# Kernel tuning notes

Measured on AMD Instinct MI355X. Metric: run time of the kernel, lower is better.

The kernel has to match this reference:

```python
import jax, jax.numpy as jnp
import numpy as np

DECAY = 0.99
EPS_VQ = 1e-5
EPS_LN = 1e-5


def setup_inputs() -> dict:
    key = jax.random.key(0)
    ks = jax.random.split(key, 6)
    N, DIN, D, K = 32768, 1024, 512, 1024
    return {
        "x": jax.random.normal(ks[0], (N, DIN), dtype=jnp.float32),
        "enc_w": jax.random.normal(ks[1], (DIN, D), dtype=jnp.float32) * (1.0 / np.sqrt(DIN)),
        "enc_b": jnp.zeros((D,), jnp.float32),
        "ln_g": jnp.ones((D,), jnp.float32),
        "ln_b": jnp.zeros((D,), jnp.float32),
        "dec_w": jax.random.normal(ks[2], (D, DIN), dtype=jnp.float32) * (1.0 / np.sqrt(D)),
        "dec_b": jnp.zeros((DIN,), jnp.float32),
        "embeddings": jax.random.normal(ks[3], (K, D), dtype=jnp.float32),
        "cluster_size": jnp.ones((K,), jnp.float32),
        "ema_embed_sum": jax.random.normal(ks[4], (K, D), dtype=jnp.float32),
    }


def _layernorm(h, g, b):
    mu = jnp.mean(h, axis=-1, keepdims=True)
    var = jnp.var(h, axis=-1, keepdims=True)
    return (h - mu) * jax.lax.rsqrt(var + EPS_LN) * g + b


def reference(x, enc_w, enc_b, ln_g, ln_b, dec_w, dec_b, embeddings, cluster_size, ema_embed_sum):
    K = embeddings.shape[0]
    # encoder: Linear + LayerNorm
    z_e = _layernorm(x @ enc_w + enc_b, ln_g, ln_b)  # [N, D]
    # pairwise squared L2 distances, expanded GEMM form (same argmin as (z-e)^2.sum)
    d = (jnp.sum(z_e * z_e, axis=1, keepdims=True)
         - 2.0 * (z_e @ embeddings.T)
         + jnp.sum(embeddings * embeddings, axis=1)[None, :])  # [N, K]
    indices = jnp.argmin(d, axis=1)  # [N]
    z_q = embeddings[indices]  # gather [N, D]
    # EMA codebook update (training path; buffers, no grad)
    zd = jax.lax.stop_gradient(z_e)
    counts = jax.ops.segment_sum(jnp.ones_like(indices, jnp.float32), indices, num_segments=K)
    embed_sum = jax.ops.segment_sum(zd, indices, num_segments=K)  # one_hot.T @ z
    new_cluster_size = DECAY * cluster_size + (1.0 - DECAY) * counts
    new_ema_embed_sum = DECAY * ema_embed_sum + (1.0 - DECAY) * embed_sum
    n = jnp.sum(new_cluster_size)
    cs = (new_cluster_size + EPS_VQ) / (n + K * EPS_VQ) * n
    new_embeddings = new_ema_embed_sum / cs[:, None]
    # commitment loss + straight-through estimator
    commit_loss = jnp.mean((z_e - jax.lax.stop_gradient(z_q)) ** 2)
    z_q_st = z_e + jax.lax.stop_gradient(z_q - z_e)
    x_recon = z_q_st @ dec_w + dec_b
    return (x_recon, commit_loss, indices, z_e, z_q_st,
            new_embeddings, new_cluster_size, new_ema_embed_sum)
```

## Files before the change

### kernel.cpp

```cpp
#include <hip/hip_runtime.h>

typedef unsigned long long u64;
typedef unsigned int u32;
typedef _Float16 f16;
typedef _Float16 f16x8 __attribute__((ext_vector_type(8)));
typedef float f32x4 __attribute__((ext_vector_type(4)));

#define MFMA16(a, b, c) __builtin_amdgcn_mfma_f32_16x16x32_f16(a, b, c, 0, 0, 0)

#define NROWS 32768
#define DIN   1024
#define DM    512
#define KC    1024
#define SPLIT_SC  1024.0f
#define SPLIT_INV 0.0009765625f
#define CHSZ  32
#define MAXCH 2048
#define MARGIN 0.5f

#define OFF_XR   0ull
#define OFF_CL   33554432ull
#define OFF_IDX  33554433ull
#define OFF_ZE   33587201ull
#define OFF_ZQ   50364417ull
#define OFF_NE   67141633ull
#define OFF_NCS  67665921ull
#define OFF_NEMA 67666945ull

#define WS_ZNORM   2359296ull
#define WS_IDX     2490368ull
#define WS_COUNTS  2621440ull
#define WS_STARTS  2625536ull
#define WS_OFFW    2629632ull
#define WS_ROWLIST 2633728ull
#define WS_CSD     2764800ull
#define WS_ENORM   2769920ull
#define WS2_CAND   (4ull<<20)
#define WS2_WT1    (36ull<<20)
#define WS2_WT2    (37ull<<20)
#define WS2_DT     (38ull<<20)
#define WS2_E1     (39ull<<20)
#define WS3_CHPFX  (41ull<<20)
#define WS3_CHCODE ((41ull<<20) + 8192)
#define WS3_CPART  ((41ull<<20) + 16384)
#define WS3_PART   ((41ull<<20) + 65536)

__device__ inline void gload16(const f16* g, f16* l) {
  __builtin_amdgcn_global_load_lds((const __attribute__((address_space(1))) void*)g,
                                   (__attribute__((address_space(3))) void*)l, 16, 0, 0);
}

__device__ inline f16x8 ldfrag32(const f16* p, int row, int kc) {
  return *(const f16x8*)(p + row * 32 + ((kc ^ ((row >> 1) & 3)) << 3));
}
__device__ inline f16x8 ldfrag64(const f16* p, int row, int kc) {
  return *(const f16x8*)(p + row * 64 + ((kc ^ (row & 7)) << 3));
}

__device__ inline void stage32(const f16* gbase, int ld, int row0, int k0,
                               f16* lds, int t) {
  int r = t >> 2, c = t & 3;
  int cs = c ^ ((r >> 1) & 3);
  gload16(gbase + (size_t)(row0 + r) * ld + k0 + cs * 8, lds + t * 8);
}

__device__ inline void stage64(const f16* gbase, int ld, int row0, int k0,
                               f16* lds, int t) {
#pragma unroll
  for (int h = 0; h < 2; h++) {
    int e = t + h * 512;
    int r = e >> 3, c = e & 7;
    int cs = c ^ (r & 7);
    gload16(gbase + (size_t)(row0 + r) * ld + k0 + cs * 8, lds + e * 8);
  }
}

#define BAR1_V4   { asm volatile("s_waitcnt vmcnt(4)" ::: "memory"); \
                    __builtin_amdgcn_sched_barrier(0); \
                    __builtin_amdgcn_s_barrier(); \
                    asm volatile("" ::: "memory"); }
#define BAR1_V0L0 { asm volatile("s_waitcnt vmcnt(0) lgkmcnt(0)" ::: "memory"); \
                    __builtin_amdgcn_sched_barrier(0); \
                    __builtin_amdgcn_s_barrier(); \
                    asm volatile("" ::: "memory"); }
#define BAR2      { asm volatile("s_waitcnt lgkmcnt(0)" ::: "memory"); \
                    __builtin_amdgcn_s_barrier(); \
                    asm volatile("" ::: "memory"); }

__device__ inline u32 enc_score(float s) {
  u32 kb = __float_as_uint(s);
  return (kb & 0x80000000u) ? ~kb : (kb | 0x80000000u);
}
__device__ inline float dec_score(u32 u) {
  u32 b = (u & 0x80000000u) ? (u & 0x7fffffffu) : ~u;
  return __uint_as_float(b);
}

__global__ __launch_bounds__(256) void k_prep(const float* __restrict__ enc_w,
                                              const float* __restrict__ dec_w,
                                              const float* __restrict__ emb,
                                              f16* __restrict__ wt1,
                                              f16* __restrict__ wt2,
                                              f16* __restrict__ dT,
                                              f16* __restrict__ e1,
                                              float* __restrict__ enorm,
                                              int* __restrict__ counts) {
  __shared__ float tile[32][33];
  int bid = blockIdx.x, t = threadIdx.x;
  if (bid < 1024) {
    const float* W;
    f16 *o1, *o2;
    int K, N, bx, by;
    if (bid < 512) {
      W = enc_w; o1 = wt1; o2 = wt2; K = DIN; N = DM;
      bx = bid & 15; by = bid >> 4;
    } else {
      int b2 = bid - 512;
      W = dec_w; o1 = dT; o2 = nullptr; K = DM; N = DIN;
      bx = b2 & 31; by = b2 >> 5;
    }
    int tx = t & 31, ty = t >> 5;
    int nb = bx * 32, kb = by * 32;
#pragma unroll
    for (int i = 0; i < 32; i += 8)
      tile[ty + i][tx] = W[(size_t)(kb + ty + i) * N + nb + tx];
    __syncthreads();
#pragma unroll
    for (int i = 0; i < 32; i += 8) {
      float v = tile[tx][ty + i];
      f16 h = (f16)v;
      size_t o = (size_t)(nb + ty + i) * K + kb + tx;
      o1[o] = h;
      if (o2) o2[o] = (f16)((v - (float)h) * SPLIT_SC);
    }
  } else if (bid < 1536) {
    int tid = (bid - 1024) * 256 + t;
    for (int i = tid; i < KC * DM; i += 131072) e1[i] = (f16)emb[i];
  } else if (bid < 1792) {
    int k = (bid - 1536) * 4 + (t >> 6), lane = t & 63;
    float s = 0.f;
#pragma unroll
    for (int j = 0; j < 8; j++) {
      float v = emb[(size_t)k * DM + lane + j * 64];
      s = fmaf(v, v, s);
    }
#pragma unroll
    for (int m = 1; m < 64; m <<= 1) s += __shfl_xor(s, m, 64);
    if (lane == 0) enorm[k] = s;
  } else {
    int i = (bid - 1792) * 256 + t;
    if (i < KC) counts[i] = 0;
  }
}

__global__ __launch_bounds__(512) void k_genc4(const float* __restrict__ x,
                                               const f16* __restrict__ wt1,
                                               const f16* __restrict__ wt2,
                                               const float* __restrict__ bias,
                                               float* __restrict__ dst) {
  __shared__ __align__(16) f16 A1[128 * 32], A2[128 * 32];
  __shared__ __align__(16) f16 B1[2][128 * 32], B2[2][128 * 32];
  int t = threadIdx.x, lane = t & 63, wid = t >> 6;
  int wm = wid >> 2, wn = wid & 3;
  int l = blockIdx.x;
  int xcd = l & 7, s = l >> 3, ct = s & 3;
  int p = ((s >> 2) << 3) | xcd;
  int m0 = p * 128, n0 = ct * 128;
  int r = t >> 2, cg = t & 3;
  int cslot = cg ^ ((r >> 1) & 3);
  const float* ax = x + (size_t)(m0 + r) * DIN + cg * 8;
  f32x4 accA[4][2] = {}, accB[4][2] = {};

#define GCONV(v0, v1)                                                       \
  {                                                                         \
    float a_[8] = {v0.x, v0.y, v0.z, v0.w, v1.x, v1.y, v1.z, v1.w};         \
    f16 h1_[8], h2_[8];                                                     \
    _Pragma("unroll") for (int j_ = 0; j_ < 8; j_++) {                      \
      f16 h_ = (f16)a_[j_];                                                 \
      h1_[j_] = h_;                                                         \
      h2_[j_] = (f16)((a_[j_] - (float)h_) * SPLIT_SC);                     \
    }                                                                       \
    *(f16x8*)(A1 + r * 32 + cslot * 8) = *(f16x8*)h1_;                      \
    *(f16x8*)(A2 + r * 32 + cslot * 8) = *(f16x8*)h2_;                      \
  }

#define GCOMP(buf)                                                          \
  {                                                                         \
    int kc_ = lane >> 4;                                                    \
    f16x8 a1f[4], a2f[4], b1f[2], b2f[2];                                   \
    _Pragma("unroll") for (int m_ = 0; m_ < 4; m_++) {                      \
      int row_ = wm * 64 + m_ * 16 + (lane & 15);                           \
      a1f[m_] = ldfrag32(A1, row_, kc_);                                    \
      a2f[m_] = ldfrag32(A2, row_, kc_);                                    \
    }                                                                       \
    _Pragma("unroll") for (int n_ = 0; n_ < 2; n_++) {                      \
      int row_ = wn * 32 + n_ * 16 + (lane & 15);                           \
      b1f[n_] = ldfrag32(B1[buf], row_, kc_);                               \
      b2f[n_] = ldfrag32(B2[buf], row_, kc_);                               \
    }                                                                       \
    _Pragma("unroll") for (int m_ = 0; m_ < 4; m_++)                        \
      _Pragma("unroll") for (int n_ = 0; n_ < 2; n_++) {                    \
        accA[m_][n_] = MFMA16(a1f[m_], b1f[n_], accA[m_][n_]);              \
        accB[m_][n_] = MFMA16(a1f[m_], b2f[n_], accB[m_][n_]);              \
        accB[m_][n_] = MFMA16(a2f[m_], b1f[n_], accB[m_][n_]);              \
      }                                                                     \
  }

  float4 c0 = *(const float4*)(ax);
  float4 c1 = *(const float4*)(ax + 4);
  float4 n0v = *(const float4*)(ax + 32);
  float4 n1v = *(const float4*)(ax + 36);
  stage32(wt1, DIN, n0, 0, B1[0], t);
  stage32(wt2, DIN, n0, 0, B2[0], t);
  asm volatile("s_waitcnt vmcnt(4)" ::: "memory");

  for (int it = 0; it < 32; ++it) {
    GCONV(c0, c1);
    if (it + 1 < 32) {
      stage32(wt1, DIN, n0, (it + 1) * 32, B1[(it + 1) & 1], t);
      stage32(wt2, DIN, n0, (it + 1) * 32, B2[(it + 1) & 1], t);
    }
    float4 f0, f1;
    if (it + 2 < 32) {
      f0 = *(const float4*)(ax + (it + 2) * 32);
      f1 = *(const float4*)(ax + (it + 2) * 32 + 4);
    }
    if (it <= 29) {
      asm volatile("s_waitcnt vmcnt(4) lgkmcnt(0)" ::: "memory");
    } else if (it == 30) {
      asm volatile("s_waitcnt vmcnt(2) lgkmcnt(0)" ::: "memory");
    } else {
      asm volatile("s_waitcnt vmcnt(0) lgkmcnt(0)" ::: "memory");
    }
    __builtin_amdgcn_sched_barrier(0);
    __builtin_amdgcn_s_barrier();
    asm volatile("" ::: "memory");
    GCOMP(it & 1);
    BAR2;
    c0 = n0v; c1 = n1v; n0v = f0; n1v = f1;
  }
#undef GCONV
#undef GCOMP

#pragma unroll
  for (int m = 0; m < 4; m++)
#pragma unroll
    for (int n = 0; n < 2; n++)
#pragma unroll
      for (int j = 0; j < 4; j++) {
        int row = m0 + wm * 64 + m * 16 + (lane >> 4) * 4 + j;
        int col = n0 + wn * 32 + n * 16 + (lane & 15);
        dst[(size_t)row * DM + col] = accA[m][n][j] + SPLIT_INV * accB[m][n][j] + bias[col];
      }
}

__global__ __launch_bounds__(512) void k_dist3(const f16* __restrict__ z1,
                                               const f16* __restrict__ e1,
                                               const float* __restrict__ enorm,
                                               u64* __restrict__ cand) {
  __shared__ __align__(16) f16 A1[2][128 * 64], B1[2][128 * 64];
  __shared__ u64 cand_s[128][8];
  int t = threadIdx.x, lane = t & 63, wid = t >> 6;
  int wm = wid >> 2, wn = wid & 3;
  int l = blockIdx.x;
  int xcd = l & 7, s = l >> 3, ct = s & 7;
  int p = ((s >> 3) << 3) | xcd;
  int r0 = p * 128, c0 = ct * 128;
  f32x4 acc[4][2] = {};

  stage64(z1, DM, r0, 0, A1[0], t);
  stage64(e1, DM, c0, 0, B1[0], t);
  int cur = 0;

  for (int it = 0; it < 8; ++it) {
    if (it < 7) {
      int k0n = (it + 1) * 64;
      stage64(z1, DM, r0, k0n, A1[cur ^ 1], t);
      stage64(e1, DM, c0, k0n, B1[cur ^ 1], t);
      BAR1_V4;
    } else {
      BAR1_V0L0;
    }
#pragma unroll
    for (int kk = 0; kk < 2; kk++) {
      int kc = kk * 4 + (lane >> 4);
      f16x8 a1f[4], b1f[2];
#pragma unroll
      for (int m = 0; m < 4; m++)
        a1f[m] = ldfrag64(A1[cur], wm * 64 + m * 16 + (lane & 15), kc);
#pragma unroll
      for (int n = 0; n < 2; n++)
        b1f[n] = ldfrag64(B1[cur], wn * 32 + n * 16 + (lane & 15), kc);
#pragma unroll
      for (int m = 0; m < 4; m++)
#pragma unroll
        for (int n = 0; n < 2; n++) acc[m][n] = MFMA16(a1f[m], b1f[n], acc[m][n]);
    }
    BAR2;
    cur ^= 1;
  }

  float en0 = enorm[c0 + wn * 32 + (lane & 15)];
  float en1 = enorm[c0 + wn * 32 + 16 + (lane & 15)];
#pragma unroll
  for (int m = 0; m < 4; m++)
#pragma unroll
    for (int j = 0; j < 4; j++) {
      int r_l = wm * 64 + m * 16 + (lane >> 4) * 4 + j;
      int col0 = c0 + wn * 32 + (lane & 15);
      float s0 = fmaf(-2.0f, acc[m][0][j], en0);
      float s1 = fmaf(-2.0f, acc[m][1][j], en1);
      u64 k0 = ((u64)enc_score(s0) << 32) | (u32)col0;
      u64 k1 = ((u64)enc_score(s1) << 32) | (u32)(col0 + 16);
      u64 lo = k0 < k1 ? k0 : k1;
      u64 hi = k0 < k1 ? k1 : k0;
#pragma unroll
      for (int msk = 1; msk < 16; msk <<= 1) {
        u64 lo2 = __shfl_xor(lo, msk, 64);
        u64 hi2 = __shfl_xor(hi, msk, 64);
        u64 nlo = lo < lo2 ? lo : lo2;
        u64 losr = lo < lo2 ? lo2 : lo;
        u64 nh = hi < hi2 ? hi : hi2;
        hi = losr < nh ? losr : nh;
        lo = nlo;
      }
      if ((lane & 15) == 0) {
        cand_s[r_l][wn * 2] = lo;
        cand_s[r_l][wn * 2 + 1] = hi;
      }
    }
  __syncthreads();
  if (t < 128) {
    u64 b0 = ~0ull, b1 = ~0ull;
#pragma unroll
    for (int i = 0; i < 8; i++) {
      u64 k = cand_s[t][i];
      if (k < b0) { b1 = b0; b0 = k; }
      else if (k < b1) { b1 = k; }
    }
    u64* dst = cand + ((size_t)(r0 + t) * 16 + ct * 2);
    dst[0] = b0;
    dst[1] = b1;
  }
}

__global__ __launch_bounds__(256) void k_resolve(const u64* __restrict__ cand,
                                                 const float* __restrict__ znorm,
                                                 const float* __restrict__ enorm,
                                                 const float* __restrict__ emb,
                                                 float* __restrict__ out,
                                                 int* __restrict__ idxws,
                                                 int* __restrict__ counts,
                                                 float* __restrict__ cpart) {
  int t = threadIdx.x, bid = blockIdx.x;
  int r0 = bid * 16;
  __shared__ u64 key_s[256];
  __shared__ int idx_s[16];
  __shared__ float commit_s[16];
  __shared__ int flagcnt_s;
  __shared__ int flagrow_s[16];
  key_s[t] = cand[(size_t)r0 * 16 + t];
  if (t == 0) flagcnt_s = 0;
  __syncthreads();

  if (t < 16) {
    u64 best = ~0ull;
#pragma unroll
    for (int i = 0; i < 16; i++) {
      u64 k = key_s[t * 16 + i];
      best = k < best ? k : best;
    }
    float smin = dec_score((u32)(best >> 32));
    float thr = smin + MARGIN;
    int nc = 0;
#pragma unroll
    for (int i = 0; i < 16; i++)
      if (dec_score((u32)(key_s[t * 16 + i] >> 32)) <= thr) nc++;
    idx_s[t] = (int)(u32)(best & 0xffffffffull);
    commit_s[t] = znorm[r0 + t] + smin;
    if (nc > 1) {
      int pz = atomicAdd(&flagcnt_s, 1);
      flagrow_s[pz] = t;
    }
  }
  __syncthreads();

  if (t < 64) {
    int nf = flagcnt_s;
    for (int fi = 0; fi < nf; fi++) {
      int lr = flagrow_s[fi];
      int R = r0 + lr;
      u64 amin = ~0ull;
      for (int i = 0; i < 16; i++) {
        u64 k = key_s[lr * 16 + i];
        amin = k < amin ? k : amin;
      }
      float thr = dec_score((u32)(amin >> 32)) + MARGIN;
      float zn = znorm[R];
      const float* z = out + OFF_ZE + (size_t)R * DM;
      u64 bestk = ~0ull;
      for (int i = 0; i < 16; i++) {
        u64 k = key_s[lr * 16 + i];
        if (dec_score((u32)(k >> 32)) > thr) continue;
        int c = (int)(u32)(k & 0xffffffffull);
        const float* e = emb + (size_t)c * DM;
        float pdot = 0.f;
#pragma unroll
        for (int j = 0; j < 8; j++) pdot = fmaf(z[t + j * 64], e[t + j * 64], pdot);
#pragma unroll
        for (int m = 1; m < 64; m <<= 1) pdot += __shfl_xor(pdot, m, 64);
        float d = fmaf(-2.0f, pdot, zn) + enorm[c];
        u64 pk = ((u64)enc_score(d) << 32) | (u32)c;
        bestk = pk < bestk ? pk : bestk;
      }
      if (t == 0) {
        idx_s[lr] = (int)(u32)(bestk & 0xffffffffull);
        commit_s[lr] = dec_score((u32)(bestk >> 32));
      }
    }
  }
  __syncthreads();

  if (t < 16) {
    int R = r0 + t;
    int idx = idx_s[t];
    out[OFF_IDX + R] = (float)idx;
    idxws[R] = idx;
    atomicAdd(counts + idx, 1);
  }
  __syncthreads();
  for (int rr = 0; rr < 16; rr++) {
    int R = r0 + rr;
    const float* e = emb + (size_t)idx_s[rr] * DM;
    float* zq = out + OFF_ZQ + (size_t)R * DM;
#pragma unroll
    for (int j = 0; j < 2; j++) {
      int c = t + j * 256;
      zq[c] = e[c];
    }
  }
  if (t == 0) {
    float s = 0.f;
#pragma unroll
    for (int i = 0; i < 16; i++) s += commit_s[i];
    cpart[bid] = s;
  }
}

__global__ __launch_bounds__(512) void k_gdec3(const f16* __restrict__ e1,
                                               const int* __restrict__ idxws,
                                               const f16* __restrict__ dT,
                                               const float* __restrict__ bias,
                                               float* __restrict__ dst) {
  __shared__ __align__(16) f16 A1[2][128 * 64], B1[2][128 * 64];
  int t = threadIdx.x, lane = t & 63, wid = t >> 6;
  int wm = wid >> 2, wn = wid & 3;
  int l = blockIdx.x;
  int xcd = l & 7, s = l >> 3, ct = s & 7;
  int p = ((s >> 3) << 3) | xcd;
  int m0 = p * 128, n0 = ct * 128;
  f32x4 acc[4][2] = {};

  int ra = t >> 3;
  int cs = (t & 7) ^ (ra & 7);
  int ia = idxws[m0 + ra];
  int ib = idxws[m0 + 64 + ra];
  const f16* pa = e1 + (size_t)ia * DM + cs * 8;
  const f16* pb = e1 + (size_t)ib * DM + cs * 8;

  gload16(pa, A1[0] + t * 8);
  gload16(pb, A1[0] + (t + 512) * 8);
  stage64(dT, DM, n0, 0, B1[0], t);
  int cur = 0;

  for (int it = 0; it < 8; ++it) {
    if (it < 7) {
      int k0n = (it + 1) * 64;
      gload16(pa + k0n, A1[cur ^ 1] + t * 8);
      gload16(pb + k0n, A1[cur ^ 1] + (t + 512) * 8);
      stage64(dT, DM, n0, k0n, B1[cur ^ 1], t);
      BAR1_V4;
    } else {
      BAR1_V0L0;
    }
#pragma unroll
    for (int kk = 0; kk < 2; kk++) {
      int kc = kk * 4 + (lane >> 4);
      f16x8 a1f[4], b1f[2];
#pragma unroll
      for (int m = 0; m < 4; m++)
        a1f[m] = ldfrag64(A1[cur], wm * 64 + m * 16 + (lane & 15), kc);
#pragma unroll
      for (int n = 0; n < 2; n++)
        b1f[n] = ldfrag64(B1[cur], wn * 32 + n * 16 + (lane & 15), kc);
#pragma unroll
      for (int m = 0; m < 4; m++)
#pragma unroll
        for (int n = 0; n < 2; n++) acc[m][n] = MFMA16(a1f[m], b1f[n], acc[m][n]);
    }
    BAR2;
    cur ^= 1;
  }
#pragma unroll
  for (int m = 0; m < 4; m++)
#pragma unroll
    for (int n = 0; n < 2; n++)
#pragma unroll
      for (int j = 0; j < 4; j++) {
        int row = m0 + wm * 64 + m * 16 + (lane >> 4) * 4 + j;
        int col = n0 + wn * 32 + n * 16 + (lane & 15);
        dst[(size_t)row * DIN + col] = acc[m][n][j] + bias[col];
      }
}

__global__ __launch_bounds__(256) void k_ln3(float* __restrict__ ze,
                                             const float* __restrict__ g,
                                             const float* __restrict__ b,
                                             f16* __restrict__ z1,
                                             float* __restrict__ znorm) {
  int t = threadIdx.x, lane = t & 63, wid = t >> 6;
  int R = blockIdx.x * 4 + wid;
  float* row = ze + (size_t)R * DM;
  float v[8];
  float s = 0.f, sq = 0.f;
#pragma unroll
  for (int j = 0; j < 8; j++) {
    v[j] = row[lane + j * 64];
    s += v[j];
    sq = fmaf(v[j], v[j], sq);
  }
#pragma unroll
  for (int m = 1; m < 64; m <<= 1) {
    s += __shfl_xor(s, m, 64);
    sq += __shfl_xor(sq, m, 64);
  }
  float mu = s * (1.f / DM);
  float var = sq * (1.f / DM) - mu * mu;
  float rs = rsqrtf(var + 1e-5f);
  float zn = 0.f;
#pragma unroll
  for (int j = 0; j < 8; j++) {
    int c = lane + j * 64;
    float o = (v[j] - mu) * rs * g[c] + b[c];
    row[c] = o;
    z1[(size_t)R * DM + c] = (f16)o;
    zn = fmaf(o, o, zn);
  }
#pragma unroll
  for (int m = 1; m < 64; m <<= 1) zn += __shfl_xor(zn, m, 64);
  if (lane == 0) znorm[R] = zn;
}

__global__ __launch_bounds__(1024) void k_scan(const int* __restrict__ counts,
                                               const float* __restrict__ cs_in,
                                               float* __restrict__ out,
                                               int* __restrict__ starts,
                                               int* __restrict__ offw,
                                               float* __restrict__ csd,
                                               const float* __restrict__ cpart,
                                               int* __restrict__ chpfx,
                                               int* __restrict__ chcode) {
  __shared__ float f[1024];
  __shared__ int ib[1024];
  int t = threadIdx.x;
  f[t] = cpart[t] + cpart[t + 1024];
  __syncthreads();
  for (int s = 512; s > 0; s >>= 1) {
    if (t < s) f[t] += f[t + s];
    __syncthreads();
  }
  if (t == 0) out[OFF_CL] = f[0] * (1.f / ((float)NROWS * (float)DM));
  __syncthreads();

  int cnt = counts[t];
  float ncs = 0.99f * cs_in[t] + 0.01f * (float)cnt;
  out[OFF_NCS + t] = ncs;
  f[t] = ncs;
  __syncthreads();
  for (int s = 512; s > 0; s >>= 1) {
    if (t < s) f[t] += f[t + s];
    __syncthreads();
  }
  float n = f[0];
  csd[t] = (ncs + 1e-5f) / (n + (float)KC * 1e-5f) * n;
  ib[t] = cnt;
  __syncthreads();
  for (int s = 1; s < 1024; s <<= 1) {
    int y = (t >= s) ? ib[t - s] : 0;
    __syncthreads();
    ib[t] += y;
    __syncthreads();
  }
  int excl = ib[t] - cnt;
  starts[t] = excl;
  offw[t] = excl;
  int nch = (cnt + CHSZ - 1) / CHSZ;
  __syncthreads();
  ib[t] = nch;
  __syncthreads();
  for (int s = 1; s < 1024; s <<= 1) {
    int y = (t >= s) ? ib[t - s] : 0;
    __syncthreads();
    ib[t] += y;
    __syncthreads();
  }
  int chx = ib[t] - nch;
  chpfx[t] = chx;
  if (t == KC - 1) chpfx[KC] = ib[t];
  for (int j = 0; j < nch; j++) chcode[chx + j] = t;
}

__global__ __launch_bounds__(256) void k_scatter(const int* __restrict__ idxws,
                                                 int* __restrict__ offw,
                                                 int* __restrict__ rowlist) {
  int r = blockIdx.x * 256 + threadIdx.x;
  int idx = idxws[r];
  int pos = atomicAdd(offw + idx, 1);
  rowlist[pos] = r;
}

__global__ __launch_bounds__(128) void k_partsum(const int* __restrict__ chpfx,
                                                 const int* __restrict__ chcode,
                                                 const int* __restrict__ starts,
                                                 const int* __restrict__ counts,
                                                 const int* __restrict__ rowlist,
                                                 const float* __restrict__ out,
                                                 float* __restrict__ part) {
  int c = blockIdx.x, t = threadIdx.x;
  if (c >= chpfx[KC]) return;
  int code = chcode[c];
  int j = c - chpfx[code];
  int ofs = starts[code] + j * CHSZ;
  int len = min(CHSZ, counts[code] - j * CHSZ);
  __shared__ int rl[CHSZ];
  if (t < len) rl[t] = rowlist[ofs + t];
  __syncthreads();
  const float* zeb = out + OFF_ZE;
  float a0 = 0.f, a1 = 0.f, a2 = 0.f, a3 = 0.f;
  for (int i = 0; i < len; i++) {
    const float* z = zeb + (size_t)rl[i] * DM;
    a0 += z[t];
    a1 += z[t + 128];
    a2 += z[t + 256];
    a3 += z[t + 384];
  }
  float* pp = part + (size_t)c * DM;
  pp[t] = a0;
  pp[t + 128] = a1;
  pp[t + 256] = a2;
  pp[t + 384] = a3;
}

__global__ __launch_bounds__(128) void k_codesum2(const int* __restrict__ chpfx,
                                                  const float* __restrict__ part,
                                                  const float* __restrict__ ema_in,
                                                  const float* __restrict__ csd,
                                                  float* __restrict__ out) {
  int k = blockIdx.x, t = threadIdx.x;
  int base = chpfx[k], nch = chpfx[k + 1] - base;
  float a0 = 0.f, a1 = 0.f, a2 = 0.f, a3 = 0.f;
  for (int i = 0; i < nch; i++) {
    const float* pp = part + (size_t)(base + i) * DM;
    a0 += pp[t];
    a1 += pp[t + 128];
    a2 += pp[t + 256];
    a3 += pp[t + 384];
  }
  float cs = csd[k];
  float sum[4] = {a0, a1, a2, a3};
#pragma unroll
  for (int j = 0; j < 4; j++) {
    int c = t + j * 128;
    float e = 0.99f * ema_in[(size_t)k * DM + c] + 0.01f * sum[j];
    out[OFF_NEMA + (size_t)k * DM + c] = e;
    out[OFF_NE + (size_t)k * DM + c] = e / cs;
  }
}

extern "C" void kernel_launch(void* const* d_in, const int* in_sizes, int n_in,
                              void* d_out, int out_size, void* d_ws, size_t ws_size,
                              hipStream_t stream) {
  (void)in_sizes; (void)n_in; (void)out_size; (void)ws_size;
  const float* x = (const float*)d_in[0];
  const float* enc_w = (const float*)d_in[1];
  const float* enc_b = (const float*)d_in[2];
  const float* ln_g = (const float*)d_in[3];
  const float* ln_b = (const float*)d_in[4];
  const float* dec_w = (const float*)d_in[5];
  const float* dec_b = (const float*)d_in[6];
  const float* emb = (const float*)d_in[7];
  const float* cs_in = (const float*)d_in[8];
  const float* ema_in = (const float*)d_in[9];
  float* out = (float*)d_out;
  char* ws = (char*)d_ws;
  float* znorm = (float*)(ws + WS_ZNORM);
  int* idxws = (int*)(ws + WS_IDX);
  int* counts = (int*)(ws + WS_COUNTS);
  int* starts = (int*)(ws + WS_STARTS);
  int* offw = (int*)(ws + WS_OFFW);
  int* rowlist = (int*)(ws + WS_ROWLIST);
  float* csd = (float*)(ws + WS_CSD);
  float* enorm = (float*)(ws + WS_ENORM);
  u64* cand = (u64*)(ws + WS2_CAND);
  f16* wt1 = (f16*)(ws + WS2_WT1);
  f16* wt2 = (f16*)(ws + WS2_WT2);
  f16* dT = (f16*)(ws + WS2_DT);
  f16* e1 = (f16*)(ws + WS2_E1);
  int* chpfx = (int*)(ws + WS3_CHPFX);
  int* chcode = (int*)(ws + WS3_CHCODE);
  float* cpart = (float*)(ws + WS3_CPART);
  float* part = (float*)(ws + WS3_PART);
  f16* z1 = (f16*)out;

  k_prep<<<dim3(1796), dim3(256), 0, stream>>>(enc_w, dec_w, emb, wt1, wt2, dT,
                                               e1, enorm, counts);
  k_genc4<<<dim3(1024), dim3(512), 0, stream>>>(x, wt1, wt2, enc_b, out + OFF_ZE);
  k_ln3<<<dim3(8192), dim3(256), 0, stream>>>(out + OFF_ZE, ln_g, ln_b, z1, znorm);
  k_dist3<<<dim3(2048), dim3(512), 0, stream>>>(z1, e1, enorm, cand);
  k_resolve<<<dim3(2048), dim3(256), 0, stream>>>(cand, znorm, enorm, emb, out,
                                                  idxws, counts, cpart);
  k_scan<<<dim3(1), dim3(1024), 0, stream>>>(counts, cs_in, out, starts, offw, csd,
                                             cpart, chpfx, chcode);
  k_scatter<<<dim3(NROWS / 256), dim3(256), 0, stream>>>(idxws, offw, rowlist);
  k_partsum<<<dim3(MAXCH), dim3(128), 0, stream>>>(chpfx, chcode, starts, counts,
                                                   rowlist, out, part);
  k_codesum2<<<dim3(KC), dim3(128), 0, stream>>>(chpfx, part, ema_in, csd, out);
  k_gdec3<<<dim3(2048), dim3(512), 0, stream>>>(e1, idxws, dT, dec_b, out + OFF_XR);
}
```

Before: 368.6 us.

## Load encoder A fragments directly into registers, dropping shared-memory A staging

The encoder GEMM now has each wave own 16 rows across all 128 columns. Each wave loads and converts its x slice straight into MFMA A fragments in registers, so the A tiles no longer go through LDS and lgkmcnt waits on A are removed. It also sets launch_bounds occupancy to 4 waves per SIMD. In exchange, each B fragment is read from LDS by all 8 waves rather than 4, which raises LDS read traffic per MFMA, and global x loads follow the fragment layout instead of the previous coalesced pattern.

```diff
diff --git a/kernel.cpp b/kernel.cpp
--- a/kernel.cpp
+++ b/kernel.cpp
@@ -153,25 +153,23 @@
   }
 }
 
-__global__ __launch_bounds__(512) void k_genc4(const float* __restrict__ x,
-                                               const f16* __restrict__ wt1,
-                                               const f16* __restrict__ wt2,
-                                               const float* __restrict__ bias,
-                                               float* __restrict__ dst) {
-  __shared__ __align__(16) f16 A1[128 * 32], A2[128 * 32];
+__global__ __launch_bounds__(512, 4) void k_genc5(const float* __restrict__ x,
+                                                  const f16* __restrict__ wt1,
+                                                  const f16* __restrict__ wt2,
+                                                  const float* __restrict__ bias,
+                                                  float* __restrict__ dst) {
   __shared__ __align__(16) f16 B1[2][128 * 32], B2[2][128 * 32];
   int t = threadIdx.x, lane = t & 63, wid = t >> 6;
-  int wm = wid >> 2, wn = wid & 3;
   int l = blockIdx.x;
   int xcd = l & 7, s = l >> 3, ct = s & 3;
   int p = ((s >> 2) << 3) | xcd;
-  int m0 = p * 128, n0 = ct * 128;
-  int r = t >> 2, cg = t & 3;
-  int cslot = cg ^ ((r >> 1) & 3);
-  const float* ax = x + (size_t)(m0 + r) * DIN + cg * 8;
-  f32x4 accA[4][2] = {}, accB[4][2] = {};
-
-#define GCONV(v0, v1)                                                       \
+  int m0 = p * 128, nc0 = ct * 128;
+  int kc = lane >> 4;
+  const float* ax = x + (size_t)(m0 + wid * 16 + (lane & 15)) * DIN + kc * 8;
+  f32x4 accA[8] = {}, accB[8] = {};
+  f16x8 a1f, a2f;
+
+#define GCONV5(v0, v1)                                                      \
   {                                                                         \
     float a_[8] = {v0.x, v0.y, v0.z, v0.w, v1.x, v1.y, v1.z, v1.w};         \
     f16 h1_[8], h2_[8];                                                     \
@@ -180,45 +178,23 @@
       h1_[j_] = h_;                                                         \
       h2_[j_] = (f16)((a_[j_] - (float)h_) * SPLIT_SC);                     \
     }                                                                       \
-    *(f16x8*)(A1 + r * 32 + cslot * 8) = *(f16x8*)h1_;                      \
-    *(f16x8*)(A2 + r * 32 + cslot * 8) = *(f16x8*)h2_;                      \
-  }
-
-#define GCOMP(buf)                                                          \
-  {                                                                         \
-    int kc_ = lane >> 4;                                                    \
-    f16x8 a1f[4], a2f[4], b1f[2], b2f[2];                                   \
-    _Pragma("unroll") for (int m_ = 0; m_ < 4; m_++) {                      \
-      int row_ = wm * 64 + m_ * 16 + (lane & 15);                           \
-      a1f[m_] = ldfrag32(A1, row_, kc_);                                    \
-      a2f[m_] = ldfrag32(A2, row_, kc_);                                    \
-    }                                                                       \
-    _Pragma("unroll") for (int n_ = 0; n_ < 2; n_++) {                      \
-      int row_ = wn * 32 + n_ * 16 + (lane & 15);                           \
-      b1f[n_] = ldfrag32(B1[buf], row_, kc_);                               \
-      b2f[n_] = ldfrag32(B2[buf], row_, kc_);                               \
-    }                                                                       \
-    _Pragma("unroll") for (int m_ = 0; m_ < 4; m_++)                        \
-      _Pragma("unroll") for (int n_ = 0; n_ < 2; n_++) {                    \
-        accA[m_][n_] = MFMA16(a1f[m_], b1f[n_], accA[m_][n_]);              \
-        accB[m_][n_] = MFMA16(a1f[m_], b2f[n_], accB[m_][n_]);              \
-        accB[m_][n_] = MFMA16(a2f[m_], b1f[n_], accB[m_][n_]);              \
-      }                                                                     \
+    a1f = *(f16x8*)h1_;                                                     \
+    a2f = *(f16x8*)h2_;                                                     \
   }
 
   float4 c0 = *(const float4*)(ax);
   float4 c1 = *(const float4*)(ax + 4);
+  stage32(wt1, DIN, nc0, 0, B1[0], t);
+  stage32(wt2, DIN, nc0, 0, B2[0], t);
   float4 n0v = *(const float4*)(ax + 32);
   float4 n1v = *(const float4*)(ax + 36);
-  stage32(wt1, DIN, n0, 0, B1[0], t);
-  stage32(wt2, DIN, n0, 0, B2[0], t);
   asm volatile("s_waitcnt vmcnt(4)" ::: "memory");
 
   for (int it = 0; it < 32; ++it) {
-    GCONV(c0, c1);
+    GCONV5(c0, c1);
     if (it + 1 < 32) {
-      stage32(wt1, DIN, n0, (it + 1) * 32, B1[(it + 1) & 1], t);
-      stage32(wt2, DIN, n0, (it + 1) * 32, B2[(it + 1) & 1], t);
+      stage32(wt1, DIN, nc0, (it + 1) * 32, B1[(it + 1) & 1], t);
+      stage32(wt2, DIN, nc0, (it + 1) * 32, B2[(it + 1) & 1], t);
     }
     float4 f0, f1;
     if (it + 2 < 32) {
@@ -226,32 +202,40 @@
       f1 = *(const float4*)(ax + (it + 2) * 32 + 4);
     }
     if (it <= 29) {
-      asm volatile("s_waitcnt vmcnt(4) lgkmcnt(0)" ::: "memory");
+      asm volatile("s_waitcnt vmcnt(4)" ::: "memory");
     } else if (it == 30) {
-      asm volatile("s_waitcnt vmcnt(2) lgkmcnt(0)" ::: "memory");
+      asm volatile("s_waitcnt vmcnt(2)" ::: "memory");
     } else {
-      asm volatile("s_waitcnt vmcnt(0) lgkmcnt(0)" ::: "memory");
+      asm volatile("s_waitcnt vmcnt(0)" ::: "memory");
     }
     __builtin_amdgcn_sched_barrier(0);
     __builtin_amdgcn_s_barrier();
     asm volatile("" ::: "memory");
-    GCOMP(it & 1);
+    {
+      const f16* bp1 = B1[it & 1];
+      const f16* bp2 = B2[it & 1];
+#pragma unroll
+      for (int n = 0; n < 8; n++) {
+        f16x8 b1f = ldfrag32(bp1, n * 16 + (lane & 15), kc);
+        f16x8 b2f = ldfrag32(bp2, n * 16 + (lane & 15), kc);
+        accA[n] = MFMA16(a1f, b1f, accA[n]);
+        accB[n] = MFMA16(a1f, b2f, accB[n]);
+        accB[n] = MFMA16(a2f, b1f, accB[n]);
+      }
+    }
     BAR2;
     c0 = n0v; c1 = n1v; n0v = f0; n1v = f1;
   }
-#undef GCONV
-#undef GCOMP
-
-#pragma unroll
-  for (int m = 0; m < 4; m++)
-#pragma unroll
-    for (int n = 0; n < 2; n++)
-#pragma unroll
-      for (int j = 0; j < 4; j++) {
-        int row = m0 + wm * 64 + m * 16 + (lane >> 4) * 4 + j;
-        int col = n0 + wn * 32 + n * 16 + (lane & 15);
-        dst[(size_t)row * DM + col] = accA[m][n][j] + SPLIT_INV * accB[m][n][j] + bias[col];
-      }
+#undef GCONV5
+
+#pragma unroll
+  for (int n = 0; n < 8; n++)
+#pragma unroll
+    for (int j = 0; j < 4; j++) {
+      int row = m0 + wid * 16 + (lane >> 4) * 4 + j;
+      int col = nc0 + n * 16 + (lane & 15);
+      dst[(size_t)row * DM + col] = accA[n][j] + SPLIT_INV * accB[n][j] + bias[col];
+    }
 }
 
 __global__ __launch_bounds__(512) void k_dist3(const f16* __restrict__ z1,
@@ -714,7 +698,7 @@
 
   k_prep<<<dim3(1796), dim3(256), 0, stream>>>(enc_w, dec_w, emb, wt1, wt2, dT,
                                                e1, enorm, counts);
-  k_genc4<<<dim3(1024), dim3(512), 0, stream>>>(x, wt1, wt2, enc_b, out + OFF_ZE);
+  k_genc5<<<dim3(1024), dim3(512), 0, stream>>>(x, wt1, wt2, enc_b, out + OFF_ZE);
   k_ln3<<<dim3(8192), dim3(256), 0, stream>>>(out + OFF_ZE, ln_g, ln_b, z1, znorm);
   k_dist3<<<dim3(2048), dim3(512), 0, stream>>>(z1, e1, enorm, cand);
   k_resolve<<<dim3(2048), dim3(256), 0, stream>>>(cand, znorm, enorm, emb, out,
```

Measured after the change: 386.5 us. 4.8% more time.

## Use 256x128 tiles with triple-buffered k32 pipeline for distance and decoder GEMMs

Applied to the files above, without the earlier changes.

Replaces the 128x128 double-buffered distance and decoder GEMM kernels with 256x128 tiles. Each wave now computes a 64x64 sub-tile, and a three-stage LDS ring with 32-wide K steps needs only one barrier per iteration. This raises arithmetic intensity per loaded byte, halves the block count, and removes the second barrier. In exchange it uses more LDS and registers per block, which may reduce occupancy, and makes the K loop longer with less work per step.

```diff
diff --git a/kernel.cpp b/kernel.cpp
--- a/kernel.cpp
+++ b/kernel.cpp
@@ -53,9 +53,6 @@
 __device__ inline f16x8 ldfrag32(const f16* p, int row, int kc) {
   return *(const f16x8*)(p + row * 32 + ((kc ^ ((row >> 1) & 3)) << 3));
 }
-__device__ inline f16x8 ldfrag64(const f16* p, int row, int kc) {
-  return *(const f16x8*)(p + row * 64 + ((kc ^ (row & 7)) << 3));
-}
 
 __device__ inline void stage32(const f16* gbase, int ld, int row0, int k0,
                                f16* lds, int t) {
@@ -64,25 +61,17 @@
   gload16(gbase + (size_t)(row0 + r) * ld + k0 + cs * 8, lds + t * 8);
 }
 
-__device__ inline void stage64(const f16* gbase, int ld, int row0, int k0,
-                               f16* lds, int t) {
+__device__ inline void stageA256(const f16* gbase, int ld, int row0, int k0,
+                                 f16* lds, int t) {
 #pragma unroll
   for (int h = 0; h < 2; h++) {
     int e = t + h * 512;
-    int r = e >> 3, c = e & 7;
-    int cs = c ^ (r & 7);
+    int r = e >> 2, c = e & 3;
+    int cs = c ^ ((r >> 1) & 3);
     gload16(gbase + (size_t)(row0 + r) * ld + k0 + cs * 8, lds + e * 8);
   }
 }
 
-#define BAR1_V4   { asm volatile("s_waitcnt vmcnt(4)" ::: "memory"); \
-                    __builtin_amdgcn_sched_barrier(0); \
-                    __builtin_amdgcn_s_barrier(); \
-                    asm volatile("" ::: "memory"); }
-#define BAR1_V0L0 { asm volatile("s_waitcnt vmcnt(0) lgkmcnt(0)" ::: "memory"); \
-                    __builtin_amdgcn_sched_barrier(0); \
-                    __builtin_amdgcn_s_barrier(); \
-                    asm volatile("" ::: "memory"); }
 #define BAR2      { asm volatile("s_waitcnt lgkmcnt(0)" ::: "memory"); \
                     __builtin_amdgcn_s_barrier(); \
                     asm volatile("" ::: "memory"); }
@@ -254,66 +243,71 @@
       }
 }
 
-__global__ __launch_bounds__(512) void k_dist3(const f16* __restrict__ z1,
-                                               const f16* __restrict__ e1,
-                                               const float* __restrict__ enorm,
-                                               u64* __restrict__ cand) {
-  __shared__ __align__(16) f16 A1[2][128 * 64], B1[2][128 * 64];
-  __shared__ u64 cand_s[128][8];
+__global__ __launch_bounds__(512, 4) void k_dist4(const f16* __restrict__ z1,
+                                                  const f16* __restrict__ e1,
+                                                  const float* __restrict__ enorm,
+                                                  u64* __restrict__ cand) {
+  __shared__ __align__(16) f16 A[3][256 * 32];
+  __shared__ __align__(16) f16 B[3][128 * 32];
   int t = threadIdx.x, lane = t & 63, wid = t >> 6;
-  int wm = wid >> 2, wn = wid & 3;
+  int wr = wid >> 1, wc = wid & 1;
   int l = blockIdx.x;
   int xcd = l & 7, s = l >> 3, ct = s & 7;
   int p = ((s >> 3) << 3) | xcd;
-  int r0 = p * 128, c0 = ct * 128;
-  f32x4 acc[4][2] = {};
-
-  stage64(z1, DM, r0, 0, A1[0], t);
-  stage64(e1, DM, c0, 0, B1[0], t);
-  int cur = 0;
-
-  for (int it = 0; it < 8; ++it) {
-    if (it < 7) {
-      int k0n = (it + 1) * 64;
-      stage64(z1, DM, r0, k0n, A1[cur ^ 1], t);
-      stage64(e1, DM, c0, k0n, B1[cur ^ 1], t);
-      BAR1_V4;
+  int r0 = p * 256, c0 = ct * 128;
+  f32x4 acc[4][4] = {};
+  int kc = lane >> 4;
+
+  stageA256(z1, DM, r0, 0, A[0], t);
+  stage32(e1, DM, c0, 0, B[0], t);
+
+  for (int it = 0; it < 16; ++it) {
+    int buf = it % 3;
+    if (it < 15) {
+      int nb = (it + 1) % 3;
+      int k0n = (it + 1) * 32;
+      stageA256(z1, DM, r0, k0n, A[nb], t);
+      stage32(e1, DM, c0, k0n, B[nb], t);
+      asm volatile("s_waitcnt vmcnt(3)" ::: "memory");
     } else {
-      BAR1_V0L0;
-    }
-#pragma unroll
-    for (int kk = 0; kk < 2; kk++) {
-      int kc = kk * 4 + (lane >> 4);
-      f16x8 a1f[4], b1f[2];
-#pragma unroll
-      for (int m = 0; m < 4; m++)
-        a1f[m] = ldfrag64(A1[cur], wm * 64 + m * 16 + (lane & 15), kc);
-#pragma unroll
-      for (int n = 0; n < 2; n++)
-        b1f[n] = ldfrag64(B1[cur], wn * 32 + n * 16 + (lane & 15), kc);
-#pragma unroll
-      for (int m = 0; m < 4; m++)
-#pragma unroll
-        for (int n = 0; n < 2; n++) acc[m][n] = MFMA16(a1f[m], b1f[n], acc[m][n]);
-    }
-    BAR2;
-    cur ^= 1;
-  }
-
-  float en0 = enorm[c0 + wn * 32 + (lane & 15)];
-  float en1 = enorm[c0 + wn * 32 + 16 + (lane & 15)];
+      asm volatile("s_waitcnt vmcnt(0)" ::: "memory");
+    }
+    __builtin_amdgcn_sched_barrier(0);
+    __builtin_amdgcn_s_barrier();
+    asm volatile("" ::: "memory");
+    f16x8 af[4], bf[4];
+#pragma unroll
+    for (int m = 0; m < 4; m++)
+      af[m] = ldfrag32(A[buf], wr * 64 + m * 16 + (lane & 15), kc);
+#pragma unroll
+    for (int n = 0; n < 4; n++)
+      bf[n] = ldfrag32(B[buf], wc * 64 + n * 16 + (lane & 15), kc);
+#pragma unroll
+    for (int m = 0; m < 4; m++)
+#pragma unroll
+      for (int n = 0; n < 4; n++) acc[m][n] = MFMA16(af[m], bf[n], acc[m][n]);
+  }
+
+  __syncthreads();
+  u64 (*cand_s)[4] = (u64 (*)[4])(&A[0][0]);
+  float en[4];
+#pragma unroll
+  for (int n = 0; n < 4; n++)
+    en[n] = enorm[c0 + wc * 64 + n * 16 + (lane & 15)];
 #pragma unroll
   for (int m = 0; m < 4; m++)
 #pragma unroll
     for (int j = 0; j < 4; j++) {
-      int r_l = wm * 64 + m * 16 + (lane >> 4) * 4 + j;
-      int col0 = c0 + wn * 32 + (lane & 15);
-      float s0 = fmaf(-2.0f, acc[m][0][j], en0);
-      float s1 = fmaf(-2.0f, acc[m][1][j], en1);
-      u64 k0 = ((u64)enc_score(s0) << 32) | (u32)col0;
-      u64 k1 = ((u64)enc_score(s1) << 32) | (u32)(col0 + 16);
-      u64 lo = k0 < k1 ? k0 : k1;
-      u64 hi = k0 < k1 ? k1 : k0;
+      int r_l = wr * 64 + m * 16 + (lane >> 4) * 4 + j;
+      u64 lo = ~0ull, hi = ~0ull;
+#pragma unroll
+      for (int n = 0; n < 4; n++) {
+        int col = c0 + wc * 64 + n * 16 + (lane & 15);
+        float sc = fmaf(-2.0f, acc[m][n][j], en[n]);
+        u64 k = ((u64)enc_score(sc) << 32) | (u32)col;
+        if (k < lo) { hi = lo; lo = k; }
+        else if (k < hi) { hi = k; }
+      }
 #pragma unroll
       for (int msk = 1; msk < 16; msk <<= 1) {
         u64 lo2 = __shfl_xor(lo, msk, 64);
@@ -325,15 +319,15 @@
         lo = nlo;
       }
       if ((lane & 15) == 0) {
-        cand_s[r_l][wn * 2] = lo;
-        cand_s[r_l][wn * 2 + 1] = hi;
+        cand_s[r_l][wc * 2] = lo;
+        cand_s[r_l][wc * 2 + 1] = hi;
       }
     }
   __syncthreads();
-  if (t < 128) {
+  if (t < 256) {
     u64 b0 = ~0ull, b1 = ~0ull;
 #pragma unroll
-    for (int i = 0; i < 8; i++) {
+    for (int i = 0; i < 4; i++) {
       u64 k = cand_s[t][i];
       if (k < b0) { b1 = b0; b0 = k; }
       else if (k < b1) { b1 = k; }
@@ -342,6 +336,73 @@
     dst[0] = b0;
     dst[1] = b1;
   }
+}
+
+__global__ __launch_bounds__(512, 4) void k_gdec4(const f16* __restrict__ e1,
+                                                  const int* __restrict__ idxws,
+                                                  const f16* __restrict__ dT,
+                                                  const float* __restrict__ bias,
+                                                  float* __restrict__ dst) {
+  __shared__ __align__(16) f16 A[3][256 * 32];
+  __shared__ __align__(16) f16 B[3][128 * 32];
+  int t = threadIdx.x, lane = t & 63, wid = t >> 6;
+  int wr = wid >> 1, wc = wid & 1;
+  int l = blockIdx.x;
+  int xcd = l & 7, s = l >> 3, ct = s & 7;
+  int p = ((s >> 3) << 3) | xcd;
+  int r0 = p * 256, c0 = ct * 128;
+  f32x4 acc[4][4] = {};
+  int kc = lane >> 4;
+
+  int rlo = t >> 2, clo = t & 3;
+  int cs0 = clo ^ ((rlo >> 1) & 3);
+  int i0 = idxws[r0 + rlo];
+  int i1 = idxws[r0 + 128 + rlo];
+  const f16* ga0 = e1 + (size_t)i0 * DM + cs0 * 8;
+  const f16* ga1 = e1 + (size_t)i1 * DM + cs0 * 8;
+
+  gload16(ga0, A[0] + t * 8);
+  gload16(ga1, A[0] + (t + 512) * 8);
+  stage32(dT, DM, c0, 0, B[0], t);
+
+  for (int it = 0; it < 16; ++it) {
+    int buf = it % 3;
+    if (it < 15) {
+      int nb = (it + 1) % 3;
+      int k0n = (it + 1) * 32;
+      gload16(ga0 + k0n, A[nb] + t * 8);
+      gload16(ga1 + k0n, A[nb] + (t + 512) * 8);
+      stage32(dT, DM, c0, k0n, B[nb], t);
+      asm volatile("s_waitcnt vmcnt(3)" ::: "memory");
+    } else {
+      asm volatile("s_waitcnt vmcnt(0)" ::: "memory");
+    }
+    __builtin_amdgcn_sched_barrier(0);
+    __builtin_amdgcn_s_barrier();
+    asm volatile("" ::: "memory");
+    f16x8 af[4], bf[4];
+#pragma unroll
+    for (int m = 0; m < 4; m++)
+      af[m] = ldfrag32(A[buf], wr * 64 + m * 16 + (lane & 15), kc);
+#pragma unroll
+    for (int n = 0; n < 4; n++)
+      bf[n] = ldfrag32(B[buf], wc * 64 + n * 16 + (lane & 15), kc);
+#pragma unroll
+    for (int m = 0; m < 4; m++)
+#pragma unroll
+      for (int n = 0; n < 4; n++) acc[m][n] = MFMA16(af[m], bf[n], acc[m][n]);
+  }
+
+#pragma unroll
+  for (int m = 0; m < 4; m++)
+#pragma unroll
+    for (int n = 0; n < 4; n++)
+#pragma unroll
+      for (int j = 0; j < 4; j++) {
+        int row = r0 + wr * 64 + m * 16 + (lane >> 4) * 4 + j;
+        int col = c0 + wc * 64 + n * 16 + (lane & 15);
+        dst[(size_t)row * DIN + col] = acc[m][n][j] + bias[col];
+      }
 }
 
 __global__ __launch_bounds__(256) void k_resolve(const u64* __restrict__ cand,
@@ -445,72 +506,6 @@
     for (int i = 0; i < 16; i++) s += commit_s[i];
     cpart[bid] = s;
   }
-}
-
-__global__ __launch_bounds__(512) void k_gdec3(const f16* __restrict__ e1,
-                                               const int* __restrict__ idxws,
-                                               const f16* __restrict__ dT,
-                                               const float* __restrict__ bias,
-                                               float* __restrict__ dst) {
-  __shared__ __align__(16) f16 A1[2][128 * 64], B1[2][128 * 64];
-  int t = threadIdx.x, lane = t & 63, wid = t >> 6;
-  int wm = wid >> 2, wn = wid & 3;
-  int l = blockIdx.x;
-  int xcd = l & 7, s = l >> 3, ct = s & 7;
-  int p = ((s >> 3) << 3) | xcd;
-  int m0 = p * 128, n0 = ct * 128;
-  f32x4 acc[4][2] = {};
-
-  int ra = t >> 3;
-  int cs = (t & 7) ^ (ra & 7);
-  int ia = idxws[m0 + ra];
-  int ib = idxws[m0 + 64 + ra];
-  const f16* pa = e1 + (size_t)ia * DM + cs * 8;
-  const f16* pb = e1 + (size_t)ib * DM + cs * 8;
-
-  gload16(pa, A1[0] + t * 8);
-  gload16(pb, A1[0] + (t + 512) * 8);
-  stage64(dT, DM, n0, 0, B1[0], t);
-  int cur = 0;
-
-  for (int it = 0; it < 8; ++it) {
-    if (it < 7) {
-      int k0n = (it + 1) * 64;
-      gload16(pa + k0n, A1[cur ^ 1] + t * 8);
-      gload16(pb + k0n, A1[cur ^ 1] + (t + 512) * 8);
-      stage64(dT, DM, n0, k0n, B1[cur ^ 1], t);
-      BAR1_V4;
-    } else {
-      BAR1_V0L0;
-    }
-#pragma unroll
-    for (int kk = 0; kk < 2; kk++) {
-      int kc = kk * 4 + (lane >> 4);
-      f16x8 a1f[4], b1f[2];
-#pragma unroll
-      for (int m = 0; m < 4; m++)
-        a1f[m] = ldfrag64(A1[cur], wm * 64 + m * 16 + (lane & 15), kc);
-#pragma unroll
-      for (int n = 0; n < 2; n++)
-        b1f[n] = ldfrag64(B1[cur], wn * 32 + n * 16 + (lane & 15), kc);
-#pragma unroll
-      for (int m = 0; m < 4; m++)
-#pragma unroll
-        for (int n = 0; n < 2; n++) acc[m][n] = MFMA16(a1f[m], b1f[n], acc[m][n]);
-    }
-    BAR2;
-    cur ^= 1;
-  }
-#pragma unroll
-  for (int m = 0; m < 4; m++)
-#pragma unroll
-    for (int n = 0; n < 2; n++)
-#pragma unroll
-      for (int j = 0; j < 4; j++) {
-        int row = m0 + wm * 64 + m * 16 + (lane >> 4) * 4 + j;
-        int col = n0 + wn * 32 + n * 16 + (lane & 15);
-        dst[(size_t)row * DIN + col] = acc[m][n][j] + bias[col];
-      }
 }
 
 __global__ __launch_bounds__(256) void k_ln3(float* __restrict__ ze,
@@ -716,7 +711,7 @@
                                                e1, enorm, counts);
   k_genc4<<<dim3(1024), dim3(512), 0, stream>>>(x, wt1, wt2, enc_b, out + OFF_ZE);
   k_ln3<<<dim3(8192), dim3(256), 0, stream>>>(out + OFF_ZE, ln_g, ln_b, z1, znorm);
-  k_dist3<<<dim3(2048), dim3(512), 0, stream>>>(z1, e1, enorm, cand);
+  k_dist4<<<dim3(1024), dim3(512), 0, stream>>>(z1, e1, enorm, cand);
   k_resolve<<<dim3(2048), dim3(256), 0, stream>>>(cand, znorm, enorm, emb, out,
                                                   idxws, counts, cpart);
   k_scan<<<dim3(1), dim3(1024), 0, stream>>>(counts, cs_in, out, starts, offw, csd,
@@ -725,5 +720,5 @@
   k_partsum<<<dim3(MAXCH), dim3(128), 0, stream>>>(chpfx, chcode, starts, counts,
                                                    rowlist, out, part);
   k_codesum2<<<dim3(KC), dim3(128), 0, stream>>>(chpfx, part, ema_in, csd, out);
-  k_gdec3<<<dim3(2048), dim3(512), 0, stream>>>(e1, idxws, dT, dec_b, out + OFF_XR);
-}
+  k_gdec4<<<dim3(1024), dim3(512), 0, stream>>>(e1, idxws, dT, dec_b, out + OFF_XR);
+}
```

Result: faster. 343.5 us (-6.8%).
